# Kernel optimization log

Measured on AMD Instinct MI355X. Metric: run time of the kernel, lower is better.

The kernel has to match this reference:

```python
import jax, jax.numpy as jnp
import numpy as np

N_NODES = 100000


def _gcn_layer(x, src, dst, ew, norm_s, norm_d, W, b):
    # DGL GraphConv with edge weights, norm='both':
    # h_v = D_in(v)^-1/2 * sum_{(u,v) in E} w_uv * D_out(u)^-1/2 * x_u; then Linear.
    m = (x * norm_s[:, None])[src] * ew[:, None]        # [E, d] gather + weight
    agg = jax.ops.segment_sum(m, dst, num_segments=N_NODES)  # [N, d] scatter-add
    return (agg * norm_d[:, None]) @ W + b


def setup_inputs() -> dict:
    key = jax.random.key(0)
    ks = jax.random.split(key, 12)
    N, E, D, C = N_NODES, 1600000, 64, 32
    inp = {
        "x": jax.random.normal(ks[0], (N, D), jnp.float32),
        "src": jax.random.randint(ks[1], (E,), 0, N, jnp.int64),
        "dst": jax.random.randint(ks[2], (E,), 0, N, jnp.int64),
        "ew": jax.random.uniform(ks[3], (E,), jnp.float32),
    }
    s = 1.0 / np.sqrt(D)
    for i, k in zip(range(1, 5), ks[4:8]):
        inp[f"W{i}"] = jax.random.normal(k, (D, D), jnp.float32) * s
        inp[f"b{i}"] = jnp.zeros((D,), jnp.float32)
    inp["Wr"] = jax.random.normal(ks[8], (D, D), jnp.float32) * s
    inp["br"] = jnp.zeros((D,), jnp.float32)
    inp["Wo"] = jax.random.normal(ks[9], (D, C), jnp.float32) * s
    inp["bo"] = jnp.zeros((C,), jnp.float32)
    return inp


def reference(x, src, dst, ew, W1, b1, W2, b2, W3, b3, W4, b4, Wr, br, Wo, bo):
    ones = jnp.ones(src.shape, x.dtype)
    deg_out = jnp.clip(jax.ops.segment_sum(ones, src, num_segments=N_NODES), 1.0)
    deg_in = jnp.clip(jax.ops.segment_sum(ones, dst, num_segments=N_NODES), 1.0)
    norm_s = deg_out ** -0.5
    norm_d = deg_in ** -0.5

    res = x @ Wr + br
    h = jax.nn.relu(_gcn_layer(x, src, dst, ew, norm_s, norm_d, W1, b1))
    h = jax.nn.relu(_gcn_layer(h, src, dst, ew, norm_s, norm_d, W2, b2))
    h = jax.nn.relu(_gcn_layer(h, src, dst, ew, norm_s, norm_d, W3, b3))
    h = _gcn_layer(h, src, dst, ew, norm_s, norm_d, W4, b4)
    h = jax.nn.relu(h + res)
    return h @ Wo + bo
```

## Files before the change

### kernel.cpp

```cpp
#include <hip/hip_runtime.h>

#define NN 100000
#define D 64
#define G 3
#define RS 33334
#define NC 85
#define NB (G*NC)

typedef short bf16x8 __attribute__((ext_vector_type(8)));
typedef float f32x4 __attribute__((ext_vector_type(4)));
typedef float f32x2 __attribute__((ext_vector_type(2)));

__device__ __forceinline__ float bf2f_lo(unsigned w) { return __uint_as_float(w << 16); }
__device__ __forceinline__ float bf2f_hi(unsigned w) { return __uint_as_float(w & 0xffff0000u); }
__device__ __forceinline__ unsigned short f2bf(float f) {
    unsigned u = __float_as_uint(f);
    return (unsigned short)((u + 0x7fffu + ((u >> 16) & 1u)) >> 16);
}
__device__ __forceinline__ unsigned pack2(float a, float b) {
    return (unsigned)f2bf(a) | ((unsigned)f2bf(b) << 16);
}
__device__ __forceinline__ unsigned char f2fp8(float v) {
    return (unsigned char)(__builtin_amdgcn_cvt_pk_fp8_f32(v, v, 0, false) & 0xff);
}
__device__ __forceinline__ unsigned pack_cw(int s, float w) {
    return ((unsigned)f2bf(w) << 17) | (unsigned)s;
}

__global__ __launch_bounds__(1024) void k_hist(const int* __restrict__ src,
                                               const int* __restrict__ dst,
                                               unsigned short* __restrict__ psd, int E) {
    __shared__ unsigned h[RS / 2];
    int b = blockIdx.x, t = threadIdx.x;
    int g = b / NC, c = b - g * NC;
    int lo = g * RS;
    for (int i = t; i < RS / 2; i += 1024) h[i] = 0;
    __syncthreads();
    int e0 = (int)((((long long)c * E / NC)) & ~3LL);
    int e1 = (c == NC - 1) ? E : (int)((((long long)(c + 1) * E / NC)) & ~3LL);
    int m = (e1 - e0) & ~4095;
    for (int e = e0 + t * 4; e < e0 + m; e += 4096) {
        int4 s4 = *(const int4*)(src + e);
        int4 d4 = *(const int4*)(dst + e);
        int v;
        v = s4.x - lo; if ((unsigned)v < RS) atomicAdd(&h[v >> 1], 1u << ((v & 1) * 16));
        v = s4.y - lo; if ((unsigned)v < RS) atomicAdd(&h[v >> 1], 1u << ((v & 1) * 16));
        v = s4.z - lo; if ((unsigned)v < RS) atomicAdd(&h[v >> 1], 1u << ((v & 1) * 16));
        v = s4.w - lo; if ((unsigned)v < RS) atomicAdd(&h[v >> 1], 1u << ((v & 1) * 16));
        v = d4.x - lo; if ((unsigned)v < RS) atomicAdd(&h[v >> 1], 1u << ((v & 1) * 16 + 8));
        v = d4.y - lo; if ((unsigned)v < RS) atomicAdd(&h[v >> 1], 1u << ((v & 1) * 16 + 8));
        v = d4.z - lo; if ((unsigned)v < RS) atomicAdd(&h[v >> 1], 1u << ((v & 1) * 16 + 8));
        v = d4.w - lo; if ((unsigned)v < RS) atomicAdd(&h[v >> 1], 1u << ((v & 1) * 16 + 8));
    }
    for (int e = e0 + m + t; e < e1; e += 1024) {
        int v = src[e] - lo; if ((unsigned)v < RS) atomicAdd(&h[v >> 1], 1u << ((v & 1) * 16));
        v = dst[e] - lo;     if ((unsigned)v < RS) atomicAdd(&h[v >> 1], 1u << ((v & 1) * 16 + 8));
    }
    __syncthreads();
    unsigned* pb = (unsigned*)(psd + (size_t)b * RS);
    for (int i = t; i < RS / 2; i += 1024) pb[i] = h[i];
}

__global__ __launch_bounds__(1024) void k_scan1m(const unsigned short* __restrict__ psd,
                                                 float* __restrict__ ns, float* __restrict__ nd,
                                                 int* __restrict__ rowptr,
                                                 int* __restrict__ bsum, int n) {
    __shared__ int lds[1024];
    int t = threadIdx.x;
    int i = blockIdx.x * 1024 + t;
    int sv = 0, dv = 0;
    if (i < n) {
        int g = i / RS, off = i - g * RS;
        const unsigned short* p = psd + (size_t)(g * NC) * RS + off;
        #pragma unroll 5
        for (int c = 0; c < NC; ++c) {
            unsigned v = p[(size_t)c * RS];
            sv += (int)(v & 0xffu);
            dv += (int)(v >> 8);
        }
        ns[i] = rsqrtf(fmaxf((float)sv, 1.0f));
        nd[i] = rsqrtf(fmaxf((float)dv, 1.0f));
    }
    lds[t] = dv;
    __syncthreads();
    for (int off = 1; off < 1024; off <<= 1) {
        int v = lds[t];
        int a = (t >= off) ? lds[t - off] : 0;
        __syncthreads();
        lds[t] = v + a;
        __syncthreads();
    }
    if (t == 1023) bsum[blockIdx.x] = lds[1023];
    if (i < n) rowptr[i] = lds[t] - dv;
}

__global__ void k_scan3c(int* __restrict__ rowptr, const int* __restrict__ bsum,
                         const unsigned short* __restrict__ psd,
                         unsigned short* __restrict__ cur16,
                         int n, int E, int nb) {
    __shared__ int sbs[128];
    int t = threadIdx.x;
    if (t < 128) sbs[t] = (t < nb) ? bsum[t] : 0;
    __syncthreads();
    for (int off = 1; off < 128; off <<= 1) {
        int v = 0, a = 0;
        if (t < 128) { v = sbs[t]; if (t >= off) a = sbs[t - off]; }
        __syncthreads();
        if (t < 128) sbs[t] = v + a;
        __syncthreads();
    }
    int i = blockIdx.x * blockDim.x + t;
    if (i == 0) rowptr[n] = E;
    if (i >= n) return;
    int blk = i >> 10;
    int base = (blk > 0) ? sbs[blk - 1] : 0;
    int r = rowptr[i] + base;
    rowptr[i] = r;
    int g = i / RS, off = i - g * RS;
    const unsigned short* p = psd + (size_t)(g * NC) * RS + off;
    unsigned short* cp = cur16 + (size_t)(g * NC) * RS + off;
    int run = 0;
    #pragma unroll 5
    for (int c = 0; c < NC; ++c) {
        cp[(size_t)c * RS] = (unsigned short)run;
        run += (int)(p[(size_t)c * RS] >> 8);
    }
}

__global__ __launch_bounds__(1024) void k_fillsort(const int* __restrict__ src,
                                                   const int* __restrict__ dst,
                                                   const float* __restrict__ ew,
                                                   const int* __restrict__ rowptr,
                                                   const unsigned short* __restrict__ cur16,
                                                   unsigned* __restrict__ cw, int E) {
    __shared__ int cur[RS];
    int b = blockIdx.x, t = threadIdx.x;
    int g = b / NC, c = b - g * NC;
    int lo = g * RS;
    const unsigned short* c16 = cur16 + (size_t)b * RS;
    for (int i = t; i < RS; i += 1024) cur[i] = rowptr[lo + i] + (int)c16[i];
    __syncthreads();
    int e0 = (int)((((long long)c * E / NC)) & ~3LL);
    int e1 = (c == NC - 1) ? E : (int)((((long long)(c + 1) * E / NC)) & ~3LL);
    int m = (e1 - e0) & ~4095;
    for (int e = e0 + t * 4; e < e0 + m; e += 4096) {
        int4 s4 = *(const int4*)(src + e);
        int4 d4 = *(const int4*)(dst + e);
        float4 w4 = *(const float4*)(ew + e);
        int d;
        d = d4.x - lo; if ((unsigned)d < RS) { int p = atomicAdd(&cur[d], 1); cw[p] = pack_cw(s4.x, w4.x); }
        d = d4.y - lo; if ((unsigned)d < RS) { int p = atomicAdd(&cur[d], 1); cw[p] = pack_cw(s4.y, w4.y); }
        d = d4.z - lo; if ((unsigned)d < RS) { int p = atomicAdd(&cur[d], 1); cw[p] = pack_cw(s4.z, w4.z); }
        d = d4.w - lo; if ((unsigned)d < RS) { int p = atomicAdd(&cur[d], 1); cw[p] = pack_cw(s4.w, w4.w); }
    }
    for (int e = e0 + m + t; e < e1; e += 1024) {
        int d = dst[e] - lo;
        if ((unsigned)d < RS) {
            int p = atomicAdd(&cur[d], 1);
            cw[p] = pack_cw(src[e], ew[e]);
        }
    }
}

template<bool LAST>
__global__ void k_gather(const int* __restrict__ rowptr, const unsigned* __restrict__ cw,
                         const unsigned char* __restrict__ tmat,
                         const float* __restrict__ nd, const float* __restrict__ ns,
                         const float* __restrict__ bias,
                         const unsigned short* __restrict__ resb,
                         unsigned short* __restrict__ outb, int n, int E) {
    int node = blockIdx.x * (blockDim.x >> 5) + (threadIdx.x >> 5);
    int lane = threadIdx.x & 31;
    if (node >= n) return;
    int g = lane >> 3;
    int h = lane & 7;
    int beg = rowptr[node], end = rowptr[node + 1];
    float a0=0,a1=0,a2=0,a3=0,a4=0,a5=0,a6=0,a7=0;
    float c0=0,c1=0,c2=0,c3=0,c4=0,c5=0,c6=0,c7=0;
    for (int base = beg; base < end; base += 16) {
        int eA = base + g;
        int eB = eA + 4;
        int eC = eA + 8;
        int eD = eA + 12;
        unsigned cvA = cw[min(eA, E - 1)];
        unsigned cvB = cw[min(eB, E - 1)];
        unsigned cvC = cw[min(eC, E - 1)];
        unsigned cvD = cw[min(eD, E - 1)];
        float wA = (eA < end) ? __uint_as_float((cvA >> 17) << 16) : 0.f;
        float wB = (eB < end) ? __uint_as_float((cvB >> 17) << 16) : 0.f;
        float wC = (eC < end) ? __uint_as_float((cvC >> 17) << 16) : 0.f;
        float wD = (eD < end) ? __uint_as_float((cvD >> 17) << 16) : 0.f;
        uint2 rA = *((const uint2*)(tmat + (size_t)(cvA & 0x1FFFFu) * D) + h);
        uint2 rB = *((const uint2*)(tmat + (size_t)(cvB & 0x1FFFFu) * D) + h);
        uint2 rC = *((const uint2*)(tmat + (size_t)(cvC & 0x1FFFFu) * D) + h);
        uint2 rD = *((const uint2*)(tmat + (size_t)(cvD & 0x1FFFFu) * D) + h);
        f32x2 p0, p1, p2, p3;
        p0 = __builtin_amdgcn_cvt_pk_f32_fp8(rA.x, false);
        p1 = __builtin_amdgcn_cvt_pk_f32_fp8(rA.x, true);
        p2 = __builtin_amdgcn_cvt_pk_f32_fp8(rA.y, false);
        p3 = __builtin_amdgcn_cvt_pk_f32_fp8(rA.y, true);
        a0 += wA * p0.x; a1 += wA * p0.y; a2 += wA * p1.x; a3 += wA * p1.y;
        a4 += wA * p2.x; a5 += wA * p2.y; a6 += wA * p3.x; a7 += wA * p3.y;
        p0 = __builtin_amdgcn_cvt_pk_f32_fp8(rB.x, false);
        p1 = __builtin_amdgcn_cvt_pk_f32_fp8(rB.x, true);
        p2 = __builtin_amdgcn_cvt_pk_f32_fp8(rB.y, false);
        p3 = __builtin_amdgcn_cvt_pk_f32_fp8(rB.y, true);
        c0 += wB * p0.x; c1 += wB * p0.y; c2 += wB * p1.x; c3 += wB * p1.y;
        c4 += wB * p2.x; c5 += wB * p2.y; c6 += wB * p3.x; c7 += wB * p3.y;
        p0 = __builtin_amdgcn_cvt_pk_f32_fp8(rC.x, false);
        p1 = __builtin_amdgcn_cvt_pk_f32_fp8(rC.x, true);
        p2 = __builtin_amdgcn_cvt_pk_f32_fp8(rC.y, false);
        p3 = __builtin_amdgcn_cvt_pk_f32_fp8(rC.y, true);
        a0 += wC * p0.x; a1 += wC * p0.y; a2 += wC * p1.x; a3 += wC * p1.y;
        a4 += wC * p2.x; a5 += wC * p2.y; a6 += wC * p3.x; a7 += wC * p3.y;
        p0 = __builtin_amdgcn_cvt_pk_f32_fp8(rD.x, false);
        p1 = __builtin_amdgcn_cvt_pk_f32_fp8(rD.x, true);
        p2 = __builtin_amdgcn_cvt_pk_f32_fp8(rD.y, false);
        p3 = __builtin_amdgcn_cvt_pk_f32_fp8(rD.y, true);
        c0 += wD * p0.x; c1 += wD * p0.y; c2 += wD * p1.x; c3 += wD * p1.y;
        c4 += wD * p2.x; c5 += wD * p2.y; c6 += wD * p3.x; c7 += wD * p3.y;
    }
    a0 += c0; a1 += c1; a2 += c2; a3 += c3;
    a4 += c4; a5 += c5; a6 += c6; a7 += c7;
    #pragma unroll
    for (int msk = 8; msk <= 16; msk <<= 1) {
        a0 += __shfl_xor(a0, msk); a1 += __shfl_xor(a1, msk);
        a2 += __shfl_xor(a2, msk); a3 += __shfl_xor(a3, msk);
        a4 += __shfl_xor(a4, msk); a5 += __shfl_xor(a5, msk);
        a6 += __shfl_xor(a6, msk); a7 += __shfl_xor(a7, msk);
    }
    float ndv = nd[node];
    float4 b0 = *(const float4*)(bias + 8 * h);
    float4 b1 = *(const float4*)(bias + 8 * h + 4);
    float v0 = ndv * a0 + b0.x, v1 = ndv * a1 + b0.y;
    float v2 = ndv * a2 + b0.z, v3 = ndv * a3 + b0.w;
    float v4 = ndv * a4 + b1.x, v5 = ndv * a5 + b1.y;
    float v6 = ndv * a6 + b1.z, v7 = ndv * a7 + b1.w;
    if (LAST) {
        uint4 r = *((const uint4*)(resb + (size_t)node * D) + h);
        v0 += bf2f_lo(r.x); v1 += bf2f_hi(r.x);
        v2 += bf2f_lo(r.y); v3 += bf2f_hi(r.y);
        v4 += bf2f_lo(r.z); v5 += bf2f_hi(r.z);
        v6 += bf2f_lo(r.w); v7 += bf2f_hi(r.w);
    }
    v0 = fmaxf(v0, 0.f); v1 = fmaxf(v1, 0.f); v2 = fmaxf(v2, 0.f); v3 = fmaxf(v3, 0.f);
    v4 = fmaxf(v4, 0.f); v5 = fmaxf(v5, 0.f); v6 = fmaxf(v6, 0.f); v7 = fmaxf(v7, 0.f);
    if (!LAST) {
        float s = ns[node];
        v0 *= s; v1 *= s; v2 *= s; v3 *= s; v4 *= s; v5 *= s; v6 *= s; v7 *= s;
    }
    if (g == 0) {
        uint4 o = make_uint4(pack2(v0, v1), pack2(v2, v3), pack2(v4, v5), pack2(v6, v7));
        *((uint4*)(outb + (size_t)node * D) + h) = o;
    }
}

template<int OUTD, bool BIAS, bool IN_BF16, int OUTMODE, bool SCALE_STORE>
__global__ __launch_bounds__(256) void k_gemm(const void* __restrict__ in_,
                                              const float* __restrict__ W,
                                              const float* __restrict__ bias,
                                              void* __restrict__ out_,
                                              const float* __restrict__ ns,
                                              unsigned short* __restrict__ xs_out,
                                              int n) {
    constexpr int NT = OUTD / 16;
    __shared__ unsigned short WT[OUTD][72];
    int t = threadIdx.x;
    for (int i = t; i < 64 * OUTD; i += 256) {
        int k = i / OUTD, nn = i % OUTD;
        WT[nn][k] = f2bf(W[i]);
    }
    __syncthreads();
    int w = t >> 6, lane = t & 63;
    int m = lane & 15, q = lane >> 4;
    int node0 = blockIdx.x * 64 + w * 16;
    int nodeA = min(node0 + m, n - 1);
    bf16x8 afr[2];
    if (IN_BF16) {
        const unsigned short* inb = (const unsigned short*)in_ + (size_t)nodeA * D;
        #pragma unroll
        for (int kc = 0; kc < 2; ++kc) {
            union { bf16x8 v; uint4 u; } tmp;
            tmp.u = *(const uint4*)(inb + kc * 32 + q * 8);
            afr[kc] = tmp.v;
        }
    } else {
        const float* inf = (const float*)in_ + (size_t)nodeA * D;
        float sc = SCALE_STORE ? ns[nodeA] : 0.f;
        #pragma unroll
        for (int kc = 0; kc < 2; ++kc) {
            float4 f0 = *(const float4*)(inf + kc * 32 + q * 8);
            float4 f1 = *(const float4*)(inf + kc * 32 + q * 8 + 4);
            union { bf16x8 v; unsigned short u[8]; } tmp;
            tmp.u[0] = f2bf(f0.x); tmp.u[1] = f2bf(f0.y);
            tmp.u[2] = f2bf(f0.z); tmp.u[3] = f2bf(f0.w);
            tmp.u[4] = f2bf(f1.x); tmp.u[5] = f2bf(f1.y);
            tmp.u[6] = f2bf(f1.z); tmp.u[7] = f2bf(f1.w);
            afr[kc] = tmp.v;
            if (SCALE_STORE && node0 + m < n) {
                uint2 o = make_uint2(pack2(f0.x * sc, f0.y * sc), pack2(f0.z * sc, f0.w * sc));
                uint2 o2 = make_uint2(pack2(f1.x * sc, f1.y * sc), pack2(f1.z * sc, f1.w * sc));
                *((uint2*)(xs_out + (size_t)nodeA * D + kc * 32 + q * 8)) = o;
                *((uint2*)(xs_out + (size_t)nodeA * D + kc * 32 + q * 8 + 4)) = o2;
            }
        }
    }
    #pragma unroll
    for (int nt = 0; nt < NT; ++nt) {
        f32x4 acc = {0.f, 0.f, 0.f, 0.f};
        #pragma unroll
        for (int kc = 0; kc < 2; ++kc) {
            union { bf16x8 v; uint4 u; } bfr;
            bfr.u = *(const uint4*)&WT[nt * 16 + m][kc * 32 + q * 8];
            acc = __builtin_amdgcn_mfma_f32_16x16x32_bf16(afr[kc], bfr.v, acc, 0, 0, 0);
        }
        int col = nt * 16 + m;
        float bb = BIAS ? bias[col] : 0.f;
        #pragma unroll
        for (int r = 0; r < 4; ++r) {
            int node = node0 + q * 4 + r;
            if (node < n) {
                float v = acc[r] + bb;
                if (OUTMODE == 2)
                    ((unsigned char*)out_)[(size_t)node * OUTD + col] = f2fp8(v);
                else if (OUTMODE == 1)
                    ((unsigned short*)out_)[(size_t)node * OUTD + col] = f2bf(v);
                else
                    ((float*)out_)[(size_t)node * OUTD + col] = v;
            }
        }
    }
}

static inline char* align_up(char* p, size_t a) {
    return (char*)(((uintptr_t)p + a - 1) & ~(uintptr_t)(a - 1));
}

extern "C" void kernel_launch(void* const* d_in, const int* in_sizes, int n_in,
                              void* d_out, int out_size, void* d_ws, size_t ws_size,
                              hipStream_t stream) {
    const float* x   = (const float*)d_in[0];
    const int*   src = (const int*)d_in[1];
    const int*   dst = (const int*)d_in[2];
    const float* ew  = (const float*)d_in[3];
    const float* Wl[4] = {(const float*)d_in[4], (const float*)d_in[6],
                          (const float*)d_in[8], (const float*)d_in[10]};
    const float* bl[4] = {(const float*)d_in[5], (const float*)d_in[7],
                          (const float*)d_in[9], (const float*)d_in[11]};
    const float* Wr = (const float*)d_in[12];
    const float* br = (const float*)d_in[13];
    const float* Wo = (const float*)d_in[14];
    const float* bo = (const float*)d_in[15];
    float* out = (float*)d_out;

    const int N = NN;
    const int E = in_sizes[1];

    char* p = (char*)d_ws;
    float* norm_s = (float*)p;            p = align_up(p + N * 4, 256);
    float* norm_d = (float*)p;            p = align_up(p + N * 4, 256);
    int*   rowptr = (int*)p;              p = align_up(p + (size_t)(G * RS + 80) * 4, 256);
    int*   bsum   = (int*)p;              p = align_up(p + 128 * 4, 256);
    unsigned* cw  = (unsigned*)p;         p = align_up(p + (size_t)E * 4, 256);
    unsigned short* psd   = (unsigned short*)p; p = align_up(p + (size_t)NB * RS * 2, 256);
    unsigned short* cur16 = (unsigned short*)p; p = align_up(p + (size_t)NB * RS * 2, 256);
    unsigned short* resb  = (unsigned short*)p; p = align_up(p + (size_t)N * D * 2, 256);
    unsigned short* xs   = psd;
    unsigned char*  tmat = (unsigned char*)(xs + (size_t)N * D);

    k_hist<<<NB, 1024, 0, stream>>>(src, dst, psd, E);
    int nb = (N + 1023) / 1024;
    k_scan1m<<<nb, 1024, 0, stream>>>(psd, norm_s, norm_d, rowptr, bsum, N);
    k_scan3c<<<(N + 255) / 256, 256, 0, stream>>>(rowptr, bsum, psd, cur16, N, E, nb);
    k_fillsort<<<NB, 1024, 0, stream>>>(src, dst, ew, rowptr, cur16, cw, E);

    k_gemm<64, true, false, 1, true><<<(N + 63) / 64, 256, 0, stream>>>(
        x, Wr, br, resb, norm_s, xs, N);

    for (int l = 0; l < 4; ++l) {
        k_gemm<64, false, true, 2, false><<<(N + 63) / 64, 256, 0, stream>>>(
            xs, Wl[l], nullptr, tmat, nullptr, nullptr, N);
        if (l < 3) {
            k_gather<false><<<(N + 7) / 8, 256, 0, stream>>>(
                rowptr, cw, tmat, norm_d, norm_s, bl[l], nullptr, xs, N, E);
        } else {
            k_gather<true><<<(N + 7) / 8, 256, 0, stream>>>(
                rowptr, cw, tmat, norm_d, nullptr, bl[l], resb, xs, N, E);
        }
    }
    k_gemm<32, true, true, 0, false><<<(N + 63) / 64, 256, 0, stream>>>(
        xs, Wo, bo, out, nullptr, nullptr, N);
}
```

Measured before the change: 331.7 us.

## Fuse gather aggregation with next-layer GEMM and merge residual/first-layer GEMMs

Each gather kernel now stages its 64 aggregated node rows in shared memory as bf16 and immediately applies the next layer's weight matrix with MFMA, writing fp8 transformed features (or the final fp32 output). The residual projection and first-layer transform are merged into one kernel that reads x once. The intent is to drop the separate GEMM launches and the bf16 intermediate round-trips through global memory, using ping-pong fp8 buffers instead. In exchange, each block handles 64 nodes serially per half-wave (8 nodes each), which cuts the number of blocks in flight and may reduce latency hiding in the gather.

```diff
diff --git a/kernel.cpp b/kernel.cpp
--- a/kernel.cpp
+++ b/kernel.cpp
@@ -162,149 +162,191 @@
     }
 }
 
-template<bool LAST>
-__global__ void k_gather(const int* __restrict__ rowptr, const unsigned* __restrict__ cw,
-                         const unsigned char* __restrict__ tmat,
-                         const float* __restrict__ nd, const float* __restrict__ ns,
-                         const float* __restrict__ bias,
-                         const unsigned short* __restrict__ resb,
-                         unsigned short* __restrict__ outb, int n, int E) {
-    int node = blockIdx.x * (blockDim.x >> 5) + (threadIdx.x >> 5);
-    int lane = threadIdx.x & 31;
-    if (node >= n) return;
-    int g = lane >> 3;
-    int h = lane & 7;
-    int beg = rowptr[node], end = rowptr[node + 1];
-    float a0=0,a1=0,a2=0,a3=0,a4=0,a5=0,a6=0,a7=0;
-    float c0=0,c1=0,c2=0,c3=0,c4=0,c5=0,c6=0,c7=0;
-    for (int base = beg; base < end; base += 16) {
-        int eA = base + g;
-        int eB = eA + 4;
-        int eC = eA + 8;
-        int eD = eA + 12;
-        unsigned cvA = cw[min(eA, E - 1)];
-        unsigned cvB = cw[min(eB, E - 1)];
-        unsigned cvC = cw[min(eC, E - 1)];
-        unsigned cvD = cw[min(eD, E - 1)];
-        float wA = (eA < end) ? __uint_as_float((cvA >> 17) << 16) : 0.f;
-        float wB = (eB < end) ? __uint_as_float((cvB >> 17) << 16) : 0.f;
-        float wC = (eC < end) ? __uint_as_float((cvC >> 17) << 16) : 0.f;
-        float wD = (eD < end) ? __uint_as_float((cvD >> 17) << 16) : 0.f;
-        uint2 rA = *((const uint2*)(tmat + (size_t)(cvA & 0x1FFFFu) * D) + h);
-        uint2 rB = *((const uint2*)(tmat + (size_t)(cvB & 0x1FFFFu) * D) + h);
-        uint2 rC = *((const uint2*)(tmat + (size_t)(cvC & 0x1FFFFu) * D) + h);
-        uint2 rD = *((const uint2*)(tmat + (size_t)(cvD & 0x1FFFFu) * D) + h);
-        f32x2 p0, p1, p2, p3;
-        p0 = __builtin_amdgcn_cvt_pk_f32_fp8(rA.x, false);
-        p1 = __builtin_amdgcn_cvt_pk_f32_fp8(rA.x, true);
-        p2 = __builtin_amdgcn_cvt_pk_f32_fp8(rA.y, false);
-        p3 = __builtin_amdgcn_cvt_pk_f32_fp8(rA.y, true);
-        a0 += wA * p0.x; a1 += wA * p0.y; a2 += wA * p1.x; a3 += wA * p1.y;
-        a4 += wA * p2.x; a5 += wA * p2.y; a6 += wA * p3.x; a7 += wA * p3.y;
-        p0 = __builtin_amdgcn_cvt_pk_f32_fp8(rB.x, false);
-        p1 = __builtin_amdgcn_cvt_pk_f32_fp8(rB.x, true);
-        p2 = __builtin_amdgcn_cvt_pk_f32_fp8(rB.y, false);
-        p3 = __builtin_amdgcn_cvt_pk_f32_fp8(rB.y, true);
-        c0 += wB * p0.x; c1 += wB * p0.y; c2 += wB * p1.x; c3 += wB * p1.y;
-        c4 += wB * p2.x; c5 += wB * p2.y; c6 += wB * p3.x; c7 += wB * p3.y;
-        p0 = __builtin_amdgcn_cvt_pk_f32_fp8(rC.x, false);
-        p1 = __builtin_amdgcn_cvt_pk_f32_fp8(rC.x, true);
-        p2 = __builtin_amdgcn_cvt_pk_f32_fp8(rC.y, false);
-        p3 = __builtin_amdgcn_cvt_pk_f32_fp8(rC.y, true);
-        a0 += wC * p0.x; a1 += wC * p0.y; a2 += wC * p1.x; a3 += wC * p1.y;
-        a4 += wC * p2.x; a5 += wC * p2.y; a6 += wC * p3.x; a7 += wC * p3.y;
-        p0 = __builtin_amdgcn_cvt_pk_f32_fp8(rD.x, false);
-        p1 = __builtin_amdgcn_cvt_pk_f32_fp8(rD.x, true);
-        p2 = __builtin_amdgcn_cvt_pk_f32_fp8(rD.y, false);
-        p3 = __builtin_amdgcn_cvt_pk_f32_fp8(rD.y, true);
-        c0 += wD * p0.x; c1 += wD * p0.y; c2 += wD * p1.x; c3 += wD * p1.y;
-        c4 += wD * p2.x; c5 += wD * p2.y; c6 += wD * p3.x; c7 += wD * p3.y;
-    }
-    a0 += c0; a1 += c1; a2 += c2; a3 += c3;
-    a4 += c4; a5 += c5; a6 += c6; a7 += c7;
+__global__ __launch_bounds__(256) void k_gemm2(const float* __restrict__ x,
+                                               const float* __restrict__ Wr,
+                                               const float* __restrict__ brs,
+                                               const float* __restrict__ W1,
+                                               const float* __restrict__ ns,
+                                               unsigned short* __restrict__ resb,
+                                               unsigned char* __restrict__ tmat, int n) {
+    __shared__ unsigned short WTr[64][72];
+    __shared__ unsigned short WT1[64][72];
+    int t = threadIdx.x;
+    for (int i = t; i < 64 * 64; i += 256) {
+        int k = i >> 6, nn = i & 63;
+        WTr[nn][k] = f2bf(Wr[i]);
+        WT1[nn][k] = f2bf(W1[i]);
+    }
+    __syncthreads();
+    int w = t >> 6, lane = t & 63;
+    int m = lane & 15, q = lane >> 4;
+    int node0 = blockIdx.x * 64 + w * 16;
+    int nodeA = min(node0 + m, n - 1);
+    const float* inf = x + (size_t)nodeA * D;
+    float sc = ns[nodeA];
+    bf16x8 afr[2], afs[2];
     #pragma unroll
-    for (int msk = 8; msk <= 16; msk <<= 1) {
-        a0 += __shfl_xor(a0, msk); a1 += __shfl_xor(a1, msk);
-        a2 += __shfl_xor(a2, msk); a3 += __shfl_xor(a3, msk);
-        a4 += __shfl_xor(a4, msk); a5 += __shfl_xor(a5, msk);
-        a6 += __shfl_xor(a6, msk); a7 += __shfl_xor(a7, msk);
-    }
-    float ndv = nd[node];
-    float4 b0 = *(const float4*)(bias + 8 * h);
-    float4 b1 = *(const float4*)(bias + 8 * h + 4);
-    float v0 = ndv * a0 + b0.x, v1 = ndv * a1 + b0.y;
-    float v2 = ndv * a2 + b0.z, v3 = ndv * a3 + b0.w;
-    float v4 = ndv * a4 + b1.x, v5 = ndv * a5 + b1.y;
-    float v6 = ndv * a6 + b1.z, v7 = ndv * a7 + b1.w;
-    if (LAST) {
-        uint4 r = *((const uint4*)(resb + (size_t)node * D) + h);
-        v0 += bf2f_lo(r.x); v1 += bf2f_hi(r.x);
-        v2 += bf2f_lo(r.y); v3 += bf2f_hi(r.y);
-        v4 += bf2f_lo(r.z); v5 += bf2f_hi(r.z);
-        v6 += bf2f_lo(r.w); v7 += bf2f_hi(r.w);
-    }
-    v0 = fmaxf(v0, 0.f); v1 = fmaxf(v1, 0.f); v2 = fmaxf(v2, 0.f); v3 = fmaxf(v3, 0.f);
-    v4 = fmaxf(v4, 0.f); v5 = fmaxf(v5, 0.f); v6 = fmaxf(v6, 0.f); v7 = fmaxf(v7, 0.f);
-    if (!LAST) {
-        float s = ns[node];
-        v0 *= s; v1 *= s; v2 *= s; v3 *= s; v4 *= s; v5 *= s; v6 *= s; v7 *= s;
-    }
-    if (g == 0) {
-        uint4 o = make_uint4(pack2(v0, v1), pack2(v2, v3), pack2(v4, v5), pack2(v6, v7));
-        *((uint4*)(outb + (size_t)node * D) + h) = o;
-    }
-}
-
-template<int OUTD, bool BIAS, bool IN_BF16, int OUTMODE, bool SCALE_STORE>
-__global__ __launch_bounds__(256) void k_gemm(const void* __restrict__ in_,
-                                              const float* __restrict__ W,
-                                              const float* __restrict__ bias,
-                                              void* __restrict__ out_,
-                                              const float* __restrict__ ns,
-                                              unsigned short* __restrict__ xs_out,
-                                              int n) {
-    constexpr int NT = OUTD / 16;
+    for (int kc = 0; kc < 2; ++kc) {
+        float4 f0 = *(const float4*)(inf + kc * 32 + q * 8);
+        float4 f1 = *(const float4*)(inf + kc * 32 + q * 8 + 4);
+        union { bf16x8 v; unsigned short u[8]; } ta, ts;
+        ta.u[0] = f2bf(f0.x); ta.u[1] = f2bf(f0.y);
+        ta.u[2] = f2bf(f0.z); ta.u[3] = f2bf(f0.w);
+        ta.u[4] = f2bf(f1.x); ta.u[5] = f2bf(f1.y);
+        ta.u[6] = f2bf(f1.z); ta.u[7] = f2bf(f1.w);
+        ts.u[0] = f2bf(f0.x * sc); ts.u[1] = f2bf(f0.y * sc);
+        ts.u[2] = f2bf(f0.z * sc); ts.u[3] = f2bf(f0.w * sc);
+        ts.u[4] = f2bf(f1.x * sc); ts.u[5] = f2bf(f1.y * sc);
+        ts.u[6] = f2bf(f1.z * sc); ts.u[7] = f2bf(f1.w * sc);
+        afr[kc] = ta.v;
+        afs[kc] = ts.v;
+    }
+    #pragma unroll
+    for (int nt = 0; nt < 4; ++nt) {
+        f32x4 ar = {0.f, 0.f, 0.f, 0.f};
+        f32x4 at = {0.f, 0.f, 0.f, 0.f};
+        #pragma unroll
+        for (int kc = 0; kc < 2; ++kc) {
+            union { bf16x8 v; uint4 u; } bfr, bf1;
+            bfr.u = *(const uint4*)&WTr[nt * 16 + m][kc * 32 + q * 8];
+            bf1.u = *(const uint4*)&WT1[nt * 16 + m][kc * 32 + q * 8];
+            ar = __builtin_amdgcn_mfma_f32_16x16x32_bf16(afr[kc], bfr.v, ar, 0, 0, 0);
+            at = __builtin_amdgcn_mfma_f32_16x16x32_bf16(afs[kc], bf1.v, at, 0, 0, 0);
+        }
+        int col = nt * 16 + m;
+        float bb = brs[col];
+        #pragma unroll
+        for (int r = 0; r < 4; ++r) {
+            int node = node0 + q * 4 + r;
+            if (node < n) {
+                resb[(size_t)node * D + col] = f2bf(ar[r] + bb);
+                tmat[(size_t)node * D + col] = f2fp8(at[r]);
+            }
+        }
+    }
+}
+
+template<int OUTD, bool LAST>
+__global__ __launch_bounds__(256) void k_gg(const int* __restrict__ rowptr,
+                                            const unsigned* __restrict__ cw,
+                                            const unsigned char* __restrict__ tmat,
+                                            const float* __restrict__ nd,
+                                            const float* __restrict__ ns,
+                                            const float* __restrict__ bg,
+                                            const unsigned short* __restrict__ resb,
+                                            const float* __restrict__ W,
+                                            const float* __restrict__ bo,
+                                            void* __restrict__ out_, int n, int E) {
+    __shared__ unsigned short HT[64][72];
     __shared__ unsigned short WT[OUTD][72];
     int t = threadIdx.x;
     for (int i = t; i < 64 * OUTD; i += 256) {
         int k = i / OUTD, nn = i % OUTD;
         WT[nn][k] = f2bf(W[i]);
     }
-    __syncthreads();
-    int w = t >> 6, lane = t & 63;
-    int m = lane & 15, q = lane >> 4;
-    int node0 = blockIdx.x * 64 + w * 16;
-    int nodeA = min(node0 + m, n - 1);
+    int hw = t >> 5;
+    int lane = t & 31;
+    int g = lane >> 3;
+    int h = lane & 7;
+    int base = blockIdx.x * 64;
+    for (int p = 0; p < 8; ++p) {
+        int nl = hw * 8 + p;
+        int node = base + nl;
+        float v0 = 0, v1 = 0, v2 = 0, v3 = 0, v4 = 0, v5 = 0, v6 = 0, v7 = 0;
+        if (node < n) {
+            int beg = rowptr[node], end = rowptr[node + 1];
+            float a0=0,a1=0,a2=0,a3=0,a4=0,a5=0,a6=0,a7=0;
+            float c0=0,c1=0,c2=0,c3=0,c4=0,c5=0,c6=0,c7=0;
+            for (int eb = beg; eb < end; eb += 16) {
+                int eA = eb + g;
+                int eB = eA + 4;
+                int eC = eA + 8;
+                int eD = eA + 12;
+                unsigned cvA = cw[min(eA, E - 1)];
+                unsigned cvB = cw[min(eB, E - 1)];
+                unsigned cvC = cw[min(eC, E - 1)];
+                unsigned cvD = cw[min(eD, E - 1)];
+                float wA = (eA < end) ? __uint_as_float((cvA >> 17) << 16) : 0.f;
+                float wB = (eB < end) ? __uint_as_float((cvB >> 17) << 16) : 0.f;
+                float wC = (eC < end) ? __uint_as_float((cvC >> 17) << 16) : 0.f;
+                float wD = (eD < end) ? __uint_as_float((cvD >> 17) << 16) : 0.f;
+                uint2 rA = *((const uint2*)(tmat + (size_t)(cvA & 0x1FFFFu) * D) + h);
+                uint2 rB = *((const uint2*)(tmat + (size_t)(cvB & 0x1FFFFu) * D) + h);
+                uint2 rC = *((const uint2*)(tmat + (size_t)(cvC & 0x1FFFFu) * D) + h);
+                uint2 rD = *((const uint2*)(tmat + (size_t)(cvD & 0x1FFFFu) * D) + h);
+                f32x2 p0, p1, p2, p3;
+                p0 = __builtin_amdgcn_cvt_pk_f32_fp8(rA.x, false);
+                p1 = __builtin_amdgcn_cvt_pk_f32_fp8(rA.x, true);
+                p2 = __builtin_amdgcn_cvt_pk_f32_fp8(rA.y, false);
+                p3 = __builtin_amdgcn_cvt_pk_f32_fp8(rA.y, true);
+                a0 += wA * p0.x; a1 += wA * p0.y; a2 += wA * p1.x; a3 += wA * p1.y;
+                a4 += wA * p2.x; a5 += wA * p2.y; a6 += wA * p3.x; a7 += wA * p3.y;
+                p0 = __builtin_amdgcn_cvt_pk_f32_fp8(rB.x, false);
+                p1 = __builtin_amdgcn_cvt_pk_f32_fp8(rB.x, true);
+                p2 = __builtin_amdgcn_cvt_pk_f32_fp8(rB.y, false);
+                p3 = __builtin_amdgcn_cvt_pk_f32_fp8(rB.y, true);
+                c0 += wB * p0.x; c1 += wB * p0.y; c2 += wB * p1.x; c3 += wB * p1.y;
+                c4 += wB * p2.x; c5 += wB * p2.y; c6 += wB * p3.x; c7 += wB * p3.y;
+                p0 = __builtin_amdgcn_cvt_pk_f32_fp8(rC.x, false);
+                p1 = __builtin_amdgcn_cvt_pk_f32_fp8(rC.x, true);
+                p2 = __builtin_amdgcn_cvt_pk_f32_fp8(rC.y, false);
+                p3 = __builtin_amdgcn_cvt_pk_f32_fp8(rC.y, true);
+                a0 += wC * p0.x; a1 += wC * p0.y; a2 += wC * p1.x; a3 += wC * p1.y;
+                a4 += wC * p2.x; a5 += wC * p2.y; a6 += wC * p3.x; a7 += wC * p3.y;
+                p0 = __builtin_amdgcn_cvt_pk_f32_fp8(rD.x, false);
+                p1 = __builtin_amdgcn_cvt_pk_f32_fp8(rD.x, true);
+                p2 = __builtin_amdgcn_cvt_pk_f32_fp8(rD.y, false);
+                p3 = __builtin_amdgcn_cvt_pk_f32_fp8(rD.y, true);
+                c0 += wD * p0.x; c1 += wD * p0.y; c2 += wD * p1.x; c3 += wD * p1.y;
+                c4 += wD * p2.x; c5 += wD * p2.y; c6 += wD * p3.x; c7 += wD * p3.y;
+            }
+            a0 += c0; a1 += c1; a2 += c2; a3 += c3;
+            a4 += c4; a5 += c5; a6 += c6; a7 += c7;
+            #pragma unroll
+            for (int msk = 8; msk <= 16; msk <<= 1) {
+                a0 += __shfl_xor(a0, msk); a1 += __shfl_xor(a1, msk);
+                a2 += __shfl_xor(a2, msk); a3 += __shfl_xor(a3, msk);
+                a4 += __shfl_xor(a4, msk); a5 += __shfl_xor(a5, msk);
+                a6 += __shfl_xor(a6, msk); a7 += __shfl_xor(a7, msk);
+            }
+            float ndv = nd[node];
+            float4 b0 = *(const float4*)(bg + 8 * h);
+            float4 b1 = *(const float4*)(bg + 8 * h + 4);
+            v0 = ndv * a0 + b0.x; v1 = ndv * a1 + b0.y;
+            v2 = ndv * a2 + b0.z; v3 = ndv * a3 + b0.w;
+            v4 = ndv * a4 + b1.x; v5 = ndv * a5 + b1.y;
+            v6 = ndv * a6 + b1.z; v7 = ndv * a7 + b1.w;
+            if (LAST) {
+                uint4 r = *((const uint4*)(resb + (size_t)node * D) + h);
+                v0 += bf2f_lo(r.x); v1 += bf2f_hi(r.x);
+                v2 += bf2f_lo(r.y); v3 += bf2f_hi(r.y);
+                v4 += bf2f_lo(r.z); v5 += bf2f_hi(r.z);
+                v6 += bf2f_lo(r.w); v7 += bf2f_hi(r.w);
+            }
+            v0 = fmaxf(v0, 0.f); v1 = fmaxf(v1, 0.f); v2 = fmaxf(v2, 0.f); v3 = fmaxf(v3, 0.f);
+            v4 = fmaxf(v4, 0.f); v5 = fmaxf(v5, 0.f); v6 = fmaxf(v6, 0.f); v7 = fmaxf(v7, 0.f);
+            if (!LAST) {
+                float s = ns[node];
+                v0 *= s; v1 *= s; v2 *= s; v3 *= s; v4 *= s; v5 *= s; v6 *= s; v7 *= s;
+            }
+        }
+        if (g == 0) {
+            *((uint4*)&HT[nl][8 * h]) =
+                make_uint4(pack2(v0, v1), pack2(v2, v3), pack2(v4, v5), pack2(v6, v7));
+        }
+    }
+    __syncthreads();
+    int w = t >> 6, l64 = t & 63;
+    int m = l64 & 15, q = l64 >> 4;
+    int row0 = w * 16;
     bf16x8 afr[2];
-    if (IN_BF16) {
-        const unsigned short* inb = (const unsigned short*)in_ + (size_t)nodeA * D;
-        #pragma unroll
-        for (int kc = 0; kc < 2; ++kc) {
-            union { bf16x8 v; uint4 u; } tmp;
-            tmp.u = *(const uint4*)(inb + kc * 32 + q * 8);
-            afr[kc] = tmp.v;
-        }
-    } else {
-        const float* inf = (const float*)in_ + (size_t)nodeA * D;
-        float sc = SCALE_STORE ? ns[nodeA] : 0.f;
-        #pragma unroll
-        for (int kc = 0; kc < 2; ++kc) {
-            float4 f0 = *(const float4*)(inf + kc * 32 + q * 8);
-            float4 f1 = *(const float4*)(inf + kc * 32 + q * 8 + 4);
-            union { bf16x8 v; unsigned short u[8]; } tmp;
-            tmp.u[0] = f2bf(f0.x); tmp.u[1] = f2bf(f0.y);
-            tmp.u[2] = f2bf(f0.z); tmp.u[3] = f2bf(f0.w);
-            tmp.u[4] = f2bf(f1.x); tmp.u[5] = f2bf(f1.y);
-            tmp.u[6] = f2bf(f1.z); tmp.u[7] = f2bf(f1.w);
-            afr[kc] = tmp.v;
-            if (SCALE_STORE && node0 + m < n) {
-                uint2 o = make_uint2(pack2(f0.x * sc, f0.y * sc), pack2(f0.z * sc, f0.w * sc));
-                uint2 o2 = make_uint2(pack2(f1.x * sc, f1.y * sc), pack2(f1.z * sc, f1.w * sc));
-                *((uint2*)(xs_out + (size_t)nodeA * D + kc * 32 + q * 8)) = o;
-                *((uint2*)(xs_out + (size_t)nodeA * D + kc * 32 + q * 8 + 4)) = o2;
-            }
-        }
-    }
+    #pragma unroll
+    for (int kc = 0; kc < 2; ++kc) {
+        union { bf16x8 v; uint4 u; } tmp;
+        tmp.u = *(const uint4*)&HT[row0 + m][kc * 32 + q * 8];
+        afr[kc] = tmp.v;
+    }
+    constexpr int NT = OUTD / 16;
     #pragma unroll
     for (int nt = 0; nt < NT; ++nt) {
         f32x4 acc = {0.f, 0.f, 0.f, 0.f};
@@ -315,18 +357,16 @@
             acc = __builtin_amdgcn_mfma_f32_16x16x32_bf16(afr[kc], bfr.v, acc, 0, 0, 0);
         }
         int col = nt * 16 + m;
-        float bb = BIAS ? bias[col] : 0.f;
+        float bb = LAST ? bo[col] : 0.f;
         #pragma unroll
         for (int r = 0; r < 4; ++r) {
-            int node = node0 + q * 4 + r;
+            int node = base + row0 + q * 4 + r;
             if (node < n) {
                 float v = acc[r] + bb;
-                if (OUTMODE == 2)
+                if (LAST)
+                    ((float*)out_)[(size_t)node * OUTD + col] = v;
+                else
                     ((unsigned char*)out_)[(size_t)node * OUTD + col] = f2fp8(v);
-                else if (OUTMODE == 1)
-                    ((unsigned short*)out_)[(size_t)node * OUTD + col] = f2bf(v);
-                else
-                    ((float*)out_)[(size_t)node * OUTD + col] = v;
             }
         }
     }
@@ -365,8 +405,8 @@
     unsigned short* psd   = (unsigned short*)p; p = align_up(p + (size_t)NB * RS * 2, 256);
     unsigned short* cur16 = (unsigned short*)p; p = align_up(p + (size_t)NB * RS * 2, 256);
     unsigned short* resb  = (unsigned short*)p; p = align_up(p + (size_t)N * D * 2, 256);
-    unsigned short* xs   = psd;
-    unsigned char*  tmat = (unsigned char*)(xs + (size_t)N * D);
+    unsigned char* tA = (unsigned char*)psd;
+    unsigned char* tB = tA + (size_t)N * D;
 
     k_hist<<<NB, 1024, 0, stream>>>(src, dst, psd, E);
     int nb = (N + 1023) / 1024;
@@ -374,20 +414,14 @@
     k_scan3c<<<(N + 255) / 256, 256, 0, stream>>>(rowptr, bsum, psd, cur16, N, E, nb);
     k_fillsort<<<NB, 1024, 0, stream>>>(src, dst, ew, rowptr, cur16, cw, E);
 
-    k_gemm<64, true, false, 1, true><<<(N + 63) / 64, 256, 0, stream>>>(
-        x, Wr, br, resb, norm_s, xs, N);
-
-    for (int l = 0; l < 4; ++l) {
-        k_gemm<64, false, true, 2, false><<<(N + 63) / 64, 256, 0, stream>>>(
-            xs, Wl[l], nullptr, tmat, nullptr, nullptr, N);
-        if (l < 3) {
-            k_gather<false><<<(N + 7) / 8, 256, 0, stream>>>(
-                rowptr, cw, tmat, norm_d, norm_s, bl[l], nullptr, xs, N, E);
-        } else {
-            k_gather<true><<<(N + 7) / 8, 256, 0, stream>>>(
-                rowptr, cw, tmat, norm_d, nullptr, bl[l], resb, xs, N, E);
-        }
-    }
-    k_gemm<32, true, true, 0, false><<<(N + 63) / 64, 256, 0, stream>>>(
-        xs, Wo, bo, out, nullptr, nullptr, N);
-}
+    k_gemm2<<<(N + 63) / 64, 256, 0, stream>>>(x, Wr, br, Wl[0], norm_s, resb, tA, N);
+
+    k_gg<64, false><<<(N + 63) / 64, 256, 0, stream>>>(
+        rowptr, cw, tA, norm_d, norm_s, bl[0], nullptr, Wl[1], nullptr, tB, N, E);
+    k_gg<64, false><<<(N + 63) / 64, 256, 0, stream>>>(
+        rowptr, cw, tB, norm_d, norm_s, bl[1], nullptr, Wl[2], nullptr, tA, N, E);
+    k_gg<64, false><<<(N + 63) / 64, 256, 0, stream>>>(
+        rowptr, cw, tA, norm_d, norm_s, bl[2], nullptr, Wl[3], nullptr, tB, N, E);
+    k_gg<32, true><<<(N + 63) / 64, 256, 0, stream>>>(
+        rowptr, cw, tB, norm_d, nullptr, bl[3], resb, Wo, bo, out, N, E);
+}
```

Result: slower. 354.8 us (+7.0%).
